# Performance work log

Measured on AMD Instinct MI355X. Metric: run time of the kernel, lower is better.

Reference implementation:

```python
import jax, jax.numpy as jnp
import numpy as np

TEMP = 0.07
POS_MARGIN = 0.1
NEG_MARGIN = 0.1
B, PM, PH, NM, NH, D = 512, 8, 16, 64, 64, 2048


def _l2(x):
    # torch F.cosine_similarity clamps norms at 1e-8
    return x / jnp.maximum(jnp.linalg.norm(x, axis=-1, keepdims=True), 1e-8)


def setup_inputs() -> dict:
    key = jax.random.key(0)
    k0, k1, k2, k3, k4 = jax.random.split(key, 5)
    return {
        "query_embeds": jax.random.normal(k0, (B, D), jnp.float32),
        "pos_main": jax.random.normal(k1, (B, PM, D), jnp.float32),
        "pos_hard": jax.random.normal(k2, (B, PH, D), jnp.float32),
        "neg_main": jax.random.normal(k3, (B, NM, D), jnp.float32),
        "neg_hard": jax.random.normal(k4, (B, NH, D), jnp.float32),
    }


def reference(query_embeds, pos_main, pos_hard, neg_main, neg_hard):
    q = _l2(query_embeds)            # [B, D]
    pm = _l2(pos_main)               # [B, PM, D]
    ph = _l2(pos_hard)               # [B, PH, D]
    nm = _l2(neg_main)               # [B, NM, D]
    nh = _l2(neg_hard)               # [B, NH, D]

    pm_sims = jnp.einsum('bd,bpd->bp', q, pm)      # [B, PM]
    anchor = pm_sims[:, 0]                          # pos_main_sims[0] per sample

    pos_score = jnp.exp(pm_sims / TEMP).sum(axis=1)
    ph_sims = jnp.einsum('bd,bpd->bp', q, ph)
    p_mask = (ph_sims >= anchor[:, None] - POS_MARGIN).astype(q.dtype)
    pos_score = pos_score + jnp.sum(p_mask * jnp.exp(ph_sims / TEMP), axis=1)

    thr = anchor[:, None] + NEG_MARGIN              # [B, 1] broadcastable threshold

    nm_sims = jnp.einsum('bd,bnd->bn', q, nm)
    neg_score = jnp.sum((nm_sims <= thr).astype(q.dtype) * jnp.exp(nm_sims / TEMP), axis=1)
    nh_sims = jnp.einsum('bd,bnd->bn', q, nh)
    neg_score = neg_score + jnp.sum((nh_sims <= thr).astype(q.dtype) * jnp.exp(nh_sims / TEMP), axis=1)

    off = 1.0 - jnp.eye(B, dtype=q.dtype)           # j != i mask

    # query_i vs query_j
    qq = q @ q.T                                    # [B, B]
    neg_score = neg_score + jnp.sum(off * (qq <= thr).astype(q.dtype) * jnp.exp(qq / TEMP), axis=1)

    pf = pm[:, 0]                                   # first positive of each sample, normalized [B, D]
    # curr_pos_i vs other_pos_j
    pp = pf @ pf.T
    neg_score = neg_score + jnp.sum(off * (pp <= thr).astype(q.dtype) * jnp.exp(pp / TEMP), axis=1)
    # query_i vs other_pos_j
    qp = q @ pf.T
    neg_score = neg_score + jnp.sum(off * (qp <= thr).astype(q.dtype) * jnp.exp(qp / TEMP), axis=1)

    loss = -jnp.log(pos_score / (pos_score + neg_score + 1e-8))
    return loss.mean()
```

## Files before the change

### kernel.cpp

```cpp
#include <hip/hip_runtime.h>
#include <math.h>

#define NB   512
#define NPM  8
#define NPH  16
#define NNM  64
#define NNH  64
#define ND   2048
#define TEMP_INV 14.285714285714285714f
#define POSM 0.1f
#define NEGM 0.1f

static constexpr int ROWS_PER_B = NPM + NPH + NNM + NNH;
static constexpr int WPB        = 8;
static constexpr int NRW        = ROWS_PER_B / WPB;

typedef __attribute__((ext_vector_type(8))) short bf16x8;
typedef __attribute__((ext_vector_type(4))) float f32x4;

__device__ __forceinline__ unsigned short f2bf(float f) {
  unsigned int u = __float_as_uint(f);
  return (unsigned short)((u + 0x7FFFu + ((u >> 16) & 1u)) >> 16);
}

__device__ __forceinline__ void acc_ss_dot(const float4 v, const float4 u,
                                           float& ss, float& dot) {
  ss  = fmaf(v.x, v.x, ss);  ss  = fmaf(v.y, v.y, ss);
  ss  = fmaf(v.z, v.z, ss);  ss  = fmaf(v.w, v.w, ss);
  dot = fmaf(v.x, u.x, dot); dot = fmaf(v.y, u.y, dot);
  dot = fmaf(v.z, u.z, dot); dot = fmaf(v.w, u.w, dot);
}

__device__ __forceinline__ void block_reduce2(float& a, float& b) {
#pragma unroll
  for (int off = 32; off > 0; off >>= 1) {
    a += __shfl_down(a, off);
    b += __shfl_down(b, off);
  }
  __shared__ float sa[4], sb[4];
  const int w = threadIdx.x >> 6;
  if ((threadIdx.x & 63) == 0) { sa[w] = a; sb[w] = b; }
  __syncthreads();
  a = sa[0] + sa[1] + sa[2] + sa[3];
  b = sb[0] + sb[1] + sb[2] + sb[3];
  __syncthreads();
}

__device__ __forceinline__ void gl_lds16(const float* g, float* l) {
  __builtin_amdgcn_global_load_lds(
      (const __attribute__((address_space(1))) unsigned int*)g,
      (__attribute__((address_space(3))) unsigned int*)l, 16, 0, 0);
}

#define VMWAIT(N) asm volatile("s_waitcnt vmcnt(" #N ")" ::: "memory")
#define ROT3()    { float* t_ = s0; s0 = s1; s1 = s2; s2 = t_; }

__global__ __launch_bounds__(256) void k_prep(const float* __restrict__ q,
                                              const float* __restrict__ pm,
                                              float* __restrict__ qn,
                                              unsigned short* __restrict__ qb,
                                              unsigned short* __restrict__ pb,
                                              float* __restrict__ anchor,
                                              float* __restrict__ pos,
                                              float* __restrict__ neg) {
  const int b = blockIdx.x;
  const int t = threadIdx.x;

  const float4* qrow = (const float4*)(q + (size_t)b * ND);
  float4 q0 = qrow[t];
  float4 q1 = qrow[t + 256];
  float ss = 0.f, dummy = 0.f;
  ss = fmaf(q0.x, q0.x, ss); ss = fmaf(q0.y, q0.y, ss);
  ss = fmaf(q0.z, q0.z, ss); ss = fmaf(q0.w, q0.w, ss);
  ss = fmaf(q1.x, q1.x, ss); ss = fmaf(q1.y, q1.y, ss);
  ss = fmaf(q1.z, q1.z, ss); ss = fmaf(q1.w, q1.w, ss);
  block_reduce2(ss, dummy);
  const float qinv = 1.0f / fmaxf(sqrtf(ss), 1e-8f);
  q0.x *= qinv; q0.y *= qinv; q0.z *= qinv; q0.w *= qinv;
  q1.x *= qinv; q1.y *= qinv; q1.z *= qinv; q1.w *= qinv;
  float4* qno = (float4*)(qn + (size_t)b * ND);
  qno[t] = q0; qno[t + 256] = q1;
  ushort4* qbo = (ushort4*)(qb + (size_t)b * ND);
  ushort4 qc0, qc1;
  qc0.x = f2bf(q0.x); qc0.y = f2bf(q0.y); qc0.z = f2bf(q0.z); qc0.w = f2bf(q0.w);
  qc1.x = f2bf(q1.x); qc1.y = f2bf(q1.y); qc1.z = f2bf(q1.z); qc1.w = f2bf(q1.w);
  qbo[t] = qc0; qbo[t + 256] = qc1;

  const float4* prow = (const float4*)(pm + (size_t)b * NPM * ND);
  float4 p0 = prow[t];
  float4 p1 = prow[t + 256];
  float pss = 0.f, dot = 0.f;
  acc_ss_dot(p0, q0, pss, dot);
  acc_ss_dot(p1, q1, pss, dot);
  block_reduce2(pss, dot);
  const float pinv = 1.0f / fmaxf(sqrtf(pss), 1e-8f);
  p0.x *= pinv; p0.y *= pinv; p0.z *= pinv; p0.w *= pinv;
  p1.x *= pinv; p1.y *= pinv; p1.z *= pinv; p1.w *= pinv;
  ushort4* pbo = (ushort4*)(pb + (size_t)b * ND);
  ushort4 pc0, pc1;
  pc0.x = f2bf(p0.x); pc0.y = f2bf(p0.y); pc0.z = f2bf(p0.z); pc0.w = f2bf(p0.w);
  pc1.x = f2bf(p1.x); pc1.y = f2bf(p1.y); pc1.z = f2bf(p1.z); pc1.w = f2bf(p1.w);
  pbo[t] = pc0; pbo[t + 256] = pc1;

  if (t == 0) {
    anchor[b] = dot * pinv;
    pos[b] = 0.f;
    neg[b] = 0.f;
  }
}

__global__ __launch_bounds__(256, 3) void k_rows(const float* __restrict__ pmain,
                                                 const float* __restrict__ phard,
                                                 const float* __restrict__ nmain,
                                                 const float* __restrict__ nhard,
                                                 const float* __restrict__ qn,
                                                 const float* __restrict__ anchor,
                                                 float* __restrict__ pos,
                                                 float* __restrict__ neg) {
  __shared__ float lds[4][3][1024];

  const int wid    = threadIdx.x >> 6;
  const int lane   = threadIdx.x & 63;
  const int wgl    = blockIdx.x * 4 + wid;
  const int b      = wgl >> 3;
  const int wslice = wgl & 7;

  auto rowbase = [&](int k) -> const float* {
    const int r = wslice + WPB * k;
    const float* p;
    if (r < NPM)                  p = pmain + ((size_t)b * NPM + r) * ND;
    else if (r < NPM + NPH)       p = phard + ((size_t)b * NPH + (r - NPM)) * ND;
    else if (r < NPM + NPH + NNM) p = nmain + ((size_t)b * NNM + (r - NPM - NPH)) * ND;
    else                          p = nhard + ((size_t)b * NNH + (r - NPM - NPH - NNM)) * ND;
    return p + lane * 4;
  };

  auto stage = [&](int c, float* slot) {
    const float* g = rowbase(c >> 1) + (c & 1) * 1024;
#pragma unroll
    for (int j = 0; j < 4; j++) gl_lds16(g + j * 256, slot + j * 256);
  };

  auto lread = [&](const float* slot, float4& A, float4& B, float4& C, float4& D) {
    const __attribute__((address_space(3))) char* ls =
        (const __attribute__((address_space(3))) char*)slot + lane * 16;
    asm volatile("ds_read_b128 %0, %4\n\t"
                 "ds_read_b128 %1, %4 offset:1024\n\t"
                 "ds_read_b128 %2, %4 offset:2048\n\t"
                 "ds_read_b128 %3, %4 offset:3072\n\t"
                 "s_waitcnt lgkmcnt(0)"
                 : "=&v"(A), "=&v"(B), "=&v"(C), "=&v"(D)
                 : "v"(ls)
                 : "memory");
    __builtin_amdgcn_sched_barrier(0);
  };

  const float4* qrow = (const float4*)(qn + (size_t)b * ND);
  const float4 u0 = qrow[lane + 64 * 0], u1 = qrow[lane + 64 * 1];
  const float4 u2 = qrow[lane + 64 * 2], u3 = qrow[lane + 64 * 3];
  const float4 u4 = qrow[lane + 64 * 4], u5 = qrow[lane + 64 * 5];
  const float4 u6 = qrow[lane + 64 * 6], u7 = qrow[lane + 64 * 7];
  const float anc = anchor[b];

  float pacc = 0.f, nacc = 0.f;

  auto finalize = [&](float ssv, float dtv, int r) {
#pragma unroll
    for (int off = 32; off > 0; off >>= 1) {
      ssv += __shfl_xor(ssv, off);
      dtv += __shfl_xor(dtv, off);
    }
    const float sim = dtv * rsqrtf(fmaxf(ssv, 1e-16f));
    const float e   = __expf(sim * TEMP_INV);
    if (r < NPM) {
      pacc += e;
    } else if (r < NPM + NPH) {
      if (sim >= anc - POSM) pacc += e;
    } else {
      if (sim <= anc + NEGM) nacc += e;
    }
  };

  float* s0 = &lds[wid][0][0];
  float* s1 = &lds[wid][1][0];
  float* s2 = &lds[wid][2][0];

  stage(0, s0); stage(1, s1); stage(2, s2);

  float4 A, B, C, D;
  for (int k = 0; k < 17; ++k) {
    float sa = 0.f, sb = 0.f, da = 0.f, db = 0.f;
    VMWAIT(8);
    lread(s0, A, B, C, D);
    stage(2 * k + 3, s0);
    ROT3();
    acc_ss_dot(A, u0, sa, da); acc_ss_dot(B, u1, sb, db);
    acc_ss_dot(C, u2, sa, da); acc_ss_dot(D, u3, sb, db);
    VMWAIT(8);
    lread(s0, A, B, C, D);
    stage(2 * k + 4, s0);
    ROT3();
    acc_ss_dot(A, u4, sa, da); acc_ss_dot(B, u5, sb, db);
    acc_ss_dot(C, u6, sa, da); acc_ss_dot(D, u7, sb, db);
    finalize(sa + sb, da + db, wslice + WPB * k);
  }
  {
    float sa = 0.f, sb = 0.f, da = 0.f, db = 0.f;
    VMWAIT(8);
    lread(s0, A, B, C, D);
    stage(37, s0);
    ROT3();
    acc_ss_dot(A, u0, sa, da); acc_ss_dot(B, u1, sb, db);
    acc_ss_dot(C, u2, sa, da); acc_ss_dot(D, u3, sb, db);
    VMWAIT(8);
    lread(s0, A, B, C, D);
    ROT3();
    acc_ss_dot(A, u4, sa, da); acc_ss_dot(B, u5, sb, db);
    acc_ss_dot(C, u6, sa, da); acc_ss_dot(D, u7, sb, db);
    finalize(sa + sb, da + db, wslice + WPB * 17);
  }
  {
    float sa = 0.f, sb = 0.f, da = 0.f, db = 0.f;
    VMWAIT(4);
    lread(s0, A, B, C, D);
    ROT3();
    acc_ss_dot(A, u0, sa, da); acc_ss_dot(B, u1, sb, db);
    acc_ss_dot(C, u2, sa, da); acc_ss_dot(D, u3, sb, db);
    VMWAIT(0);
    lread(s0, A, B, C, D);
    acc_ss_dot(A, u4, sa, da); acc_ss_dot(B, u5, sb, db);
    acc_ss_dot(C, u6, sa, da); acc_ss_dot(D, u7, sb, db);
    finalize(sa + sb, da + db, wslice + WPB * 18);
  }

  if (lane == 0) {
    if (pacc != 0.f) atomicAdd(pos + b, pacc);
    if (nacc != 0.f) atomicAdd(neg + b, nacc);
  }
}

__global__ __launch_bounds__(256) void k_sim(const unsigned short* __restrict__ qb,
                                             const unsigned short* __restrict__ pb,
                                             const float* __restrict__ anchor,
                                             float* __restrict__ neg) {
  const int z = blockIdx.z;
  const unsigned short* __restrict__ A = (z == 1) ? pb : qb;
  const unsigned short* __restrict__ B = (z == 0) ? qb : pb;

  const int wid  = blockIdx.x * 4 + (threadIdx.x >> 6);
  const int m    = wid >> 4;
  const int n2   = wid & 15;
  const int lane = threadIdx.x & 63;
  const int r16  = lane & 15;
  const int kc   = lane >> 4;

  const size_t abase  = ((size_t)(m * 16 + r16)) * ND + kc * 8;
  const size_t b0base = ((size_t)(n2 * 32 + r16)) * ND + kc * 8;
  const size_t b1base = b0base + (size_t)16 * ND;

  f32x4 acc0 = {0.f, 0.f, 0.f, 0.f};
  f32x4 acc1 = {0.f, 0.f, 0.f, 0.f};
#pragma unroll 2
  for (int k0 = 0; k0 < ND; k0 += 64) {
    const bf16x8 a0  = *(const bf16x8*)(A + abase  + k0);
    const bf16x8 a1  = *(const bf16x8*)(A + abase  + k0 + 32);
    const bf16x8 b00 = *(const bf16x8*)(B + b0base + k0);
    const bf16x8 b10 = *(const bf16x8*)(B + b1base + k0);
    const bf16x8 b01 = *(const bf16x8*)(B + b0base + k0 + 32);
    const bf16x8 b11 = *(const bf16x8*)(B + b1base + k0 + 32);
    acc0 = __builtin_amdgcn_mfma_f32_16x16x32_bf16(a0, b00, acc0, 0, 0, 0);
    acc1 = __builtin_amdgcn_mfma_f32_16x16x32_bf16(a0, b10, acc1, 0, 0, 0);
    acc0 = __builtin_amdgcn_mfma_f32_16x16x32_bf16(a1, b01, acc0, 0, 0, 0);
    acc1 = __builtin_amdgcn_mfma_f32_16x16x32_bf16(a1, b11, acc1, 0, 0, 0);
  }

  const int rbase = m * 16 + kc * 4;
  const int gc0   = n2 * 32 + r16;
#pragma unroll
  for (int j = 0; j < 4; j++) {
    const int gr = rbase + j;
    const float thr = anchor[gr] + NEGM;
    float s = 0.f;
    const float v0 = acc0[j];
    const float v1 = acc1[j];
    if (gr != gc0      && v0 <= thr) s += expf(v0 * TEMP_INV);
    if (gr != gc0 + 16 && v1 <= thr) s += expf(v1 * TEMP_INV);
    s += __shfl_xor(s, 1);
    s += __shfl_xor(s, 2);
    s += __shfl_xor(s, 4);
    s += __shfl_xor(s, 8);
    if (r16 == 0) atomicAdd(neg + gr, s);
  }
}

__global__ __launch_bounds__(512) void k_loss(const float* __restrict__ pos,
                                              const float* __restrict__ neg,
                                              float* __restrict__ out) {
  const int t = threadIdx.x;
  const float p = pos[t];
  const float n = neg[t];
  float l = -logf(p / (p + n + 1e-8f));
#pragma unroll
  for (int off = 32; off > 0; off >>= 1) l += __shfl_down(l, off);
  __shared__ float s[8];
  if ((t & 63) == 0) s[t >> 6] = l;
  __syncthreads();
  if (t == 0) {
    float tot = 0.f;
#pragma unroll
    for (int i = 0; i < 8; i++) tot += s[i];
    out[0] = tot / (float)NB;
  }
}

extern "C" void kernel_launch(void* const* d_in, const int* in_sizes, int n_in,
                              void* d_out, int out_size, void* d_ws, size_t ws_size,
                              hipStream_t stream) {
  const float* q  = (const float*)d_in[0];
  const float* pm = (const float*)d_in[1];
  const float* ph = (const float*)d_in[2];
  const float* nm = (const float*)d_in[3];
  const float* nh = (const float*)d_in[4];
  float* out = (float*)d_out;

  float* ws = (float*)d_ws;
  float*          qn     = ws;
  unsigned short* qb     = (unsigned short*)(ws + (size_t)NB * ND);
  unsigned short* pb     = qb + (size_t)NB * ND;
  float*          anchor = (float*)(pb + (size_t)NB * ND);
  float*          pos    = anchor + NB;
  float*          neg    = pos + NB;

  k_prep<<<NB, 256, 0, stream>>>(q, pm, qn, qb, pb, anchor, pos, neg);
  k_rows<<<(NB * WPB) / 4, 256, 0, stream>>>(pm, ph, nm, nh, qn, anchor, pos, neg);
  k_sim<<<dim3(128, 1, 3), 256, 0, stream>>>(qb, pb, anchor, neg);
  k_loss<<<1, 512, 0, stream>>>(pos, neg, out);
}
```

Measured before the change: 171.5 us.

## Fuse row-sim and pairwise MFMA kernels into one launch with smaller LDS stages

```diff
diff --git a/kernel.cpp b/kernel.cpp
--- a/kernel.cpp
+++ b/kernel.cpp
@@ -14,6 +14,8 @@
 static constexpr int ROWS_PER_B = NPM + NPH + NNM + NNH;
 static constexpr int WPB        = 8;
 static constexpr int NRW        = ROWS_PER_B / WPB;
+static constexpr int NBLK_ROWS  = NB * WPB / 4;
+static constexpr int NBLK_SIM   = 384;
 
 typedef __attribute__((ext_vector_type(8))) short bf16x8;
 typedef __attribute__((ext_vector_type(4))) float f32x4;
@@ -109,15 +111,71 @@
   }
 }
 
-__global__ __launch_bounds__(256, 3) void k_rows(const float* __restrict__ pmain,
+__global__ __launch_bounds__(256, 6) void k_main(const float* __restrict__ pmain,
                                                  const float* __restrict__ phard,
                                                  const float* __restrict__ nmain,
                                                  const float* __restrict__ nhard,
                                                  const float* __restrict__ qn,
+                                                 const unsigned short* __restrict__ qb,
+                                                 const unsigned short* __restrict__ pb,
                                                  const float* __restrict__ anchor,
                                                  float* __restrict__ pos,
                                                  float* __restrict__ neg) {
-  __shared__ float lds[4][3][1024];
+  __shared__ float lds[4][3][512];
+
+  if (blockIdx.x >= NBLK_ROWS) {
+    const int sblk = blockIdx.x - NBLK_ROWS;
+    const int z    = sblk >> 7;
+    const int xb   = sblk & 127;
+    const unsigned short* __restrict__ A = (z == 1) ? pb : qb;
+    const unsigned short* __restrict__ B = (z == 0) ? qb : pb;
+
+    const int wid  = xb * 4 + (threadIdx.x >> 6);
+    const int m    = wid >> 4;
+    const int n2   = wid & 15;
+    const int lane = threadIdx.x & 63;
+    const int r16  = lane & 15;
+    const int kc   = lane >> 4;
+
+    const size_t abase  = ((size_t)(m * 16 + r16)) * ND + kc * 8;
+    const size_t b0base = ((size_t)(n2 * 32 + r16)) * ND + kc * 8;
+    const size_t b1base = b0base + (size_t)16 * ND;
+
+    f32x4 acc0 = {0.f, 0.f, 0.f, 0.f};
+    f32x4 acc1 = {0.f, 0.f, 0.f, 0.f};
+#pragma unroll 2
+    for (int k0 = 0; k0 < ND; k0 += 64) {
+      const bf16x8 a0  = *(const bf16x8*)(A + abase  + k0);
+      const bf16x8 a1  = *(const bf16x8*)(A + abase  + k0 + 32);
+      const bf16x8 b00 = *(const bf16x8*)(B + b0base + k0);
+      const bf16x8 b10 = *(const bf16x8*)(B + b1base + k0);
+      const bf16x8 b01 = *(const bf16x8*)(B + b0base + k0 + 32);
+      const bf16x8 b11 = *(const bf16x8*)(B + b1base + k0 + 32);
+      acc0 = __builtin_amdgcn_mfma_f32_16x16x32_bf16(a0, b00, acc0, 0, 0, 0);
+      acc1 = __builtin_amdgcn_mfma_f32_16x16x32_bf16(a0, b10, acc1, 0, 0, 0);
+      acc0 = __builtin_amdgcn_mfma_f32_16x16x32_bf16(a1, b01, acc0, 0, 0, 0);
+      acc1 = __builtin_amdgcn_mfma_f32_16x16x32_bf16(a1, b11, acc1, 0, 0, 0);
+    }
+
+    const int rbase = m * 16 + kc * 4;
+    const int gc0   = n2 * 32 + r16;
+#pragma unroll
+    for (int j = 0; j < 4; j++) {
+      const int gr = rbase + j;
+      const float thr = anchor[gr] + NEGM;
+      float s = 0.f;
+      const float v0 = acc0[j];
+      const float v1 = acc1[j];
+      if (gr != gc0      && v0 <= thr) s += expf(v0 * TEMP_INV);
+      if (gr != gc0 + 16 && v1 <= thr) s += expf(v1 * TEMP_INV);
+      s += __shfl_xor(s, 1);
+      s += __shfl_xor(s, 2);
+      s += __shfl_xor(s, 4);
+      s += __shfl_xor(s, 8);
+      if (r16 == 0) atomicAdd(neg + gr, s);
+    }
+    return;
+  }
 
   const int wid    = threadIdx.x >> 6;
   const int lane   = threadIdx.x & 63;
@@ -136,31 +194,29 @@
   };
 
   auto stage = [&](int c, float* slot) {
-    const float* g = rowbase(c >> 1) + (c & 1) * 1024;
-#pragma unroll
-    for (int j = 0; j < 4; j++) gl_lds16(g + j * 256, slot + j * 256);
+    const float* g = rowbase(c >> 2) + (c & 3) * 512;
+    gl_lds16(g, slot);
+    gl_lds16(g + 256, slot + 256);
   };
 
-  auto lread = [&](const float* slot, float4& A, float4& B, float4& C, float4& D) {
+  auto lread2 = [&](const float* slot, float4& A, float4& B) {
     const __attribute__((address_space(3))) char* ls =
         (const __attribute__((address_space(3))) char*)slot + lane * 16;
-    asm volatile("ds_read_b128 %0, %4\n\t"
-                 "ds_read_b128 %1, %4 offset:1024\n\t"
-                 "ds_read_b128 %2, %4 offset:2048\n\t"
-                 "ds_read_b128 %3, %4 offset:3072\n\t"
+    asm volatile("ds_read_b128 %0, %2\n\t"
+                 "ds_read_b128 %1, %2 offset:1024\n\t"
                  "s_waitcnt lgkmcnt(0)"
-                 : "=&v"(A), "=&v"(B), "=&v"(C), "=&v"(D)
+                 : "=&v"(A), "=&v"(B)
                  : "v"(ls)
                  : "memory");
     __builtin_amdgcn_sched_barrier(0);
   };
 
   const float4* qrow = (const float4*)(qn + (size_t)b * ND);
-  const float4 u0 = qrow[lane + 64 * 0], u1 = qrow[lane + 64 * 1];
-  const float4 u2 = qrow[lane + 64 * 2], u3 = qrow[lane + 64 * 3];
-  const float4 u4 = qrow[lane + 64 * 4], u5 = qrow[lane + 64 * 5];
-  const float4 u6 = qrow[lane + 64 * 6], u7 = qrow[lane + 64 * 7];
+  float4 u[8];
+#pragma unroll
+  for (int j = 0; j < 8; j++) u[j] = qrow[lane + 64 * j];
   const float anc = anchor[b];
+  asm volatile("s_waitcnt vmcnt(0)" ::: "memory");
 
   float pacc = 0.f, nacc = 0.f;
 
@@ -187,109 +243,36 @@
 
   stage(0, s0); stage(1, s1); stage(2, s2);
 
-  float4 A, B, C, D;
-  for (int k = 0; k < 17; ++k) {
+  float4 A, B;
+  for (int k = 0; k < 18; ++k) {
     float sa = 0.f, sb = 0.f, da = 0.f, db = 0.f;
-    VMWAIT(8);
-    lread(s0, A, B, C, D);
-    stage(2 * k + 3, s0);
-    ROT3();
-    acc_ss_dot(A, u0, sa, da); acc_ss_dot(B, u1, sb, db);
-    acc_ss_dot(C, u2, sa, da); acc_ss_dot(D, u3, sb, db);
-    VMWAIT(8);
-    lread(s0, A, B, C, D);
-    stage(2 * k + 4, s0);
-    ROT3();
-    acc_ss_dot(A, u4, sa, da); acc_ss_dot(B, u5, sb, db);
-    acc_ss_dot(C, u6, sa, da); acc_ss_dot(D, u7, sb, db);
+#pragma unroll
+    for (int j = 0; j < 4; ++j) {
+      VMWAIT(4);
+      lread2(s0, A, B);
+      stage(4 * k + j + 3, s0);
+      ROT3();
+      acc_ss_dot(A, u[2 * j],     sa, da);
+      acc_ss_dot(B, u[2 * j + 1], sb, db);
+    }
     finalize(sa + sb, da + db, wslice + WPB * k);
   }
   {
     float sa = 0.f, sb = 0.f, da = 0.f, db = 0.f;
-    VMWAIT(8);
-    lread(s0, A, B, C, D);
-    stage(37, s0);
-    ROT3();
-    acc_ss_dot(A, u0, sa, da); acc_ss_dot(B, u1, sb, db);
-    acc_ss_dot(C, u2, sa, da); acc_ss_dot(D, u3, sb, db);
-    VMWAIT(8);
-    lread(s0, A, B, C, D);
-    ROT3();
-    acc_ss_dot(A, u4, sa, da); acc_ss_dot(B, u5, sb, db);
-    acc_ss_dot(C, u6, sa, da); acc_ss_dot(D, u7, sb, db);
-    finalize(sa + sb, da + db, wslice + WPB * 17);
-  }
-  {
-    float sa = 0.f, sb = 0.f, da = 0.f, db = 0.f;
-    VMWAIT(4);
-    lread(s0, A, B, C, D);
-    ROT3();
-    acc_ss_dot(A, u0, sa, da); acc_ss_dot(B, u1, sb, db);
-    acc_ss_dot(C, u2, sa, da); acc_ss_dot(D, u3, sb, db);
-    VMWAIT(0);
-    lread(s0, A, B, C, D);
-    acc_ss_dot(A, u4, sa, da); acc_ss_dot(B, u5, sb, db);
-    acc_ss_dot(C, u6, sa, da); acc_ss_dot(D, u7, sb, db);
+    VMWAIT(4); lread2(s0, A, B); stage(75, s0); ROT3();
+    acc_ss_dot(A, u[0], sa, da); acc_ss_dot(B, u[1], sb, db);
+    VMWAIT(4); lread2(s0, A, B); ROT3();
+    acc_ss_dot(A, u[2], sa, da); acc_ss_dot(B, u[3], sb, db);
+    VMWAIT(2); lread2(s0, A, B); ROT3();
+    acc_ss_dot(A, u[4], sa, da); acc_ss_dot(B, u[5], sb, db);
+    VMWAIT(0); lread2(s0, A, B);
+    acc_ss_dot(A, u[6], sa, da); acc_ss_dot(B, u[7], sb, db);
     finalize(sa + sb, da + db, wslice + WPB * 18);
   }
 
   if (lane == 0) {
     if (pacc != 0.f) atomicAdd(pos + b, pacc);
     if (nacc != 0.f) atomicAdd(neg + b, nacc);
-  }
-}
-
-__global__ __launch_bounds__(256) void k_sim(const unsigned short* __restrict__ qb,
-                                             const unsigned short* __restrict__ pb,
-                                             const float* __restrict__ anchor,
-                                             float* __restrict__ neg) {
-  const int z = blockIdx.z;
-  const unsigned short* __restrict__ A = (z == 1) ? pb : qb;
-  const unsigned short* __restrict__ B = (z == 0) ? qb : pb;
-
-  const int wid  = blockIdx.x * 4 + (threadIdx.x >> 6);
-  const int m    = wid >> 4;
-  const int n2   = wid & 15;
-  const int lane = threadIdx.x & 63;
-  const int r16  = lane & 15;
-  const int kc   = lane >> 4;
-
-  const size_t abase  = ((size_t)(m * 16 + r16)) * ND + kc * 8;
-  const size_t b0base = ((size_t)(n2 * 32 + r16)) * ND + kc * 8;
-  const size_t b1base = b0base + (size_t)16 * ND;
-
-  f32x4 acc0 = {0.f, 0.f, 0.f, 0.f};
-  f32x4 acc1 = {0.f, 0.f, 0.f, 0.f};
-#pragma unroll 2
-  for (int k0 = 0; k0 < ND; k0 += 64) {
-    const bf16x8 a0  = *(const bf16x8*)(A + abase  + k0);
-    const bf16x8 a1  = *(const bf16x8*)(A + abase  + k0 + 32);
-    const bf16x8 b00 = *(const bf16x8*)(B + b0base + k0);
-    const bf16x8 b10 = *(const bf16x8*)(B + b1base + k0);
-    const bf16x8 b01 = *(const bf16x8*)(B + b0base + k0 + 32);
-    const bf16x8 b11 = *(const bf16x8*)(B + b1base + k0 + 32);
-    acc0 = __builtin_amdgcn_mfma_f32_16x16x32_bf16(a0, b00, acc0, 0, 0, 0);
-    acc1 = __builtin_amdgcn_mfma_f32_16x16x32_bf16(a0, b10, acc1, 0, 0, 0);
-    acc0 = __builtin_amdgcn_mfma_f32_16x16x32_bf16(a1, b01, acc0, 0, 0, 0);
-    acc1 = __builtin_amdgcn_mfma_f32_16x16x32_bf16(a1, b11, acc1, 0, 0, 0);
-  }
-
-  const int rbase = m * 16 + kc * 4;
-  const int gc0   = n2 * 32 + r16;
-#pragma unroll
-  for (int j = 0; j < 4; j++) {
-    const int gr = rbase + j;
-    const float thr = anchor[gr] + NEGM;
-    float s = 0.f;
-    const float v0 = acc0[j];
-    const float v1 = acc1[j];
-    if (gr != gc0      && v0 <= thr) s += expf(v0 * TEMP_INV);
-    if (gr != gc0 + 16 && v1 <= thr) s += expf(v1 * TEMP_INV);
-    s += __shfl_xor(s, 1);
-    s += __shfl_xor(s, 2);
-    s += __shfl_xor(s, 4);
-    s += __shfl_xor(s, 8);
-    if (r16 == 0) atomicAdd(neg + gr, s);
   }
 }
 
@@ -332,7 +315,7 @@
   float*          neg    = pos + NB;
 
   k_prep<<<NB, 256, 0, stream>>>(q, pm, qn, qb, pb, anchor, pos, neg);
-  k_rows<<<(NB * WPB) / 4, 256, 0, stream>>>(pm, ph, nm, nh, qn, anchor, pos, neg);
-  k_sim<<<dim3(128, 1, 3), 256, 0, stream>>>(qb, pb, anchor, neg);
+  k_main<<<NBLK_ROWS + NBLK_SIM, 256, 0, stream>>>(pm, ph, nm, nh, qn, qb, pb,
+                                                   anchor, pos, neg);
   k_loss<<<1, 512, 0, stream>>>(pos, neg, out);
 }
```

Result: no change. 171.3 us (-0.1%).
